# Kernel tuning notes

Measured on AMD Instinct MI355X. Metric: run time of the kernel, lower is better.

The kernel has to match this reference:

```python
import jax, jax.numpy as jnp
import numpy as np

N, E, IN_F, EDGE_F, HID, S = 200000, 600000, 28, 4, 128, 20000
NUM_LAYERS = 4
L = NUM_LAYERS - 1
BN_EPS = 1e-5


def setup_inputs() -> dict:
    key = jax.random.key(0)
    ks = jax.random.split(key, 20)
    p = lambda k, shape: (jax.random.normal(k, shape, dtype=jnp.float32) * 0.1)
    return {
        'x': jax.random.normal(ks[0], (N, IN_F), dtype=jnp.float32),
        'edge_index': jax.random.randint(ks[1], (2, E), 0, N),
        'edge_attr': jax.random.normal(ks[2], (E, EDGE_F), dtype=jnp.float32),
        'edge_weight': jax.random.uniform(ks[3], (E,), dtype=jnp.float32),
        'node_mask': (jax.random.uniform(ks[4], (N,)) > 0.5).astype(jnp.float32),
        'subgraphs2nodes': jax.random.randint(ks[5], (N,), 0, S),
        # layer-1 params (in_features -> hidden)
        'be1_W1': p(ks[6], (EDGE_F, IN_F)), 'be1_b1': jnp.zeros((IN_F,), jnp.float32),
        'be1_W2': p(ks[7], (IN_F, IN_F)), 'be1_b2': jnp.zeros((IN_F,), jnp.float32),
        'm1_W1': p(ks[8], (IN_F, HID)), 'm1_b1': jnp.zeros((HID,), jnp.float32),
        'm1_W2': p(ks[9], (HID, HID)), 'm1_b2': jnp.zeros((HID,), jnp.float32),
        'bn1_g': jnp.ones((HID,), jnp.float32), 'bn1_b': jnp.zeros((HID,), jnp.float32),
        'eps1': jnp.zeros((), jnp.float32),
        # layers 2..NUM_LAYERS, stacked (hidden -> hidden)
        'beW1': p(ks[10], (L, EDGE_F, HID)), 'beb1': jnp.zeros((L, HID), jnp.float32),
        'beW2': p(ks[11], (L, HID, HID)), 'beb2': jnp.zeros((L, HID), jnp.float32),
        'mW1': p(ks[12], (L, HID, HID)), 'mb1': jnp.zeros((L, HID), jnp.float32),
        'mW2': p(ks[13], (L, HID, HID)), 'mb2': jnp.zeros((L, HID), jnp.float32),
        'bng': jnp.ones((L, HID), jnp.float32), 'bnb': jnp.zeros((L, HID), jnp.float32),
        'eps': jnp.zeros((L,), jnp.float32),
    }


def _mlp2(h, W1, b1, W2, b2):
    # Linear -> ReLU -> Linear
    return jnp.dot(jax.nn.relu(jnp.dot(h, W1) + b1), W2) + b2


def _gine(x, src, dst, edge_attr, edge_weight, eps,
          beW1, beb1, beW2, beb2, W1, b1, W2, b2, g, beta):
    # bond encoder on edge features
    e = _mlp2(edge_attr, beW1, beb1, beW2, beb2)            # [E, d]
    # message: relu(x_j + e_ij) * w_ij, aggregated at dst via scatter-add
    m = jax.nn.relu(x[src] + e) * edge_weight[:, None]      # [E, d]
    aggr = jax.ops.segment_sum(m, dst, num_segments=N)      # [N, d]
    h = (1.0 + eps) * x + aggr
    # node MLP: Linear,ReLU,Linear,BN(train mode),ReLU
    h = _mlp2(h, W1, b1, W2, b2)
    mu = jnp.mean(h, axis=0)
    var = jnp.mean((h - mu) ** 2, axis=0)
    h = (h - mu) * jax.lax.rsqrt(var + BN_EPS) * g + beta
    return jax.nn.relu(h)


def reference(x, edge_index, edge_attr, edge_weight, node_mask, subgraphs2nodes,
              be1_W1, be1_b1, be1_W2, be1_b2, m1_W1, m1_b1, m1_W2, m1_b2,
              bn1_g, bn1_b, eps1,
              beW1, beb1, beW2, beb2, mW1, mb1, mW2, mb2, bng, bnb, eps):
    src, dst = edge_index[0], edge_index[1]
    h = _gine(x, src, dst, edge_attr, edge_weight, eps1,
              be1_W1, be1_b1, be1_W2, be1_b2,
              m1_W1, m1_b1, m1_W2, m1_b2, bn1_g, bn1_b)
    for i in range(L):
        h_new = _gine(h, src, dst, edge_attr, edge_weight, eps[i],
                      beW1[i], beb1[i], beW2[i], beb2[i],
                      mW1[i], mb1[i], mW2[i], mb2[i], bng[i], bnb[i])
        h = h + h_new  # residual
    # float node_mask branch + global_add_pool over subgraphs2nodes
    h = h * node_mask[:, None]
    return jax.ops.segment_sum(h, subgraphs2nodes, num_segments=S)  # [S, HID]
```

## Files before the change

kernel.cpp:

```cpp
#include <hip/hip_runtime.h>
#include <hip/hip_bf16.h>


#define BNEPS 1e-5f
#define LDA 136
#define SCAN_NB 240

typedef __attribute__((ext_vector_type(8))) short bf16x8;
typedef __attribute__((ext_vector_type(8))) unsigned short u16x8;
typedef __attribute__((ext_vector_type(4))) float f32x4;

__device__ inline short f2bf(float f) {
    __hip_bfloat16 h = __float2bfloat16(f);
    return *reinterpret_cast<short*>(&h);
}
__device__ inline unsigned short f2bfu(float f) {
    __hip_bfloat16 h = __float2bfloat16(f);
    return *reinterpret_cast<unsigned short*>(&h);
}
__device__ inline float bf2f(unsigned short u) {
    union { unsigned int i; float f; } v; v.i = ((unsigned int)u) << 16; return v.f;
}


__global__ __launch_bounds__(256) void k_prep(
    const float* __restrict__ m1W2, const float* __restrict__ beW2,
    const float* __restrict__ mW1, const float* __restrict__ mW2,
    short* __restrict__ out)
{
    __shared__ float tileS[64][65];
    int b = blockIdx.x, mat = b >> 2, t = b & 3;
    const float* Wsrc;
    if (mat == 0) Wsrc = m1W2;
    else {
        int l = (mat - 1) / 3, which = (mat - 1) % 3;
        Wsrc = (which == 0) ? beW2 + (size_t)l * 16384
             : (which == 1) ? mW1 + (size_t)l * 16384
             :                mW2 + (size_t)l * 16384;
    }
    short* dst = out + (size_t)mat * 16384;
    int tr = (t >> 1) * 64, tc = (t & 1) * 64;
    for (int i = threadIdx.x; i < 4096; i += 256) {
        int r = i >> 6, c = i & 63;
        tileS[r][c] = Wsrc[(size_t)(tr + r) * 128 + (tc + c)];
    }
    __syncthreads();
    for (int i = threadIdx.x; i < 4096; i += 256) {
        int kl = i & 63, nl = i >> 6;
        int n = tc + nl, k = tr + kl;
        int fo = (((n >> 4) * 4 + (k >> 5)) * 64 + (((k >> 3) & 3) * 16 + (n & 15))) * 8 + (k & 7);
        dst[fo] = f2bf(tileS[kl][nl]);
    }
}

__global__ __launch_bounds__(256) void k_prep1(
    const float* __restrict__ W1, short* __restrict__ out)
{
    for (int i = threadIdx.x; i < 4096; i += 256) {
        int j = i & 7, sub = (i >> 3) & 63, nt = i >> 9;
        int quad = sub >> 4, l15 = sub & 15;
        int n = nt * 16 + l15, k = quad * 8 + j;
        out[i] = (k < 28) ? f2bf(W1[(size_t)k * 128 + n]) : (short)0;
    }
}

__global__ __launch_bounds__(256) void k_prep28(
    const float* __restrict__ W2, short* __restrict__ out)
{
    for (int i = threadIdx.x; i < 32 * 32; i += 256) {
        int n = i >> 5, k = i & 31;
        out[i] = (n < 28 && k < 28) ? f2bf(W2[(size_t)k * 28 + n]) : (short)0;
    }
}

__global__ __launch_bounds__(256) void k_prepx(
    const float* __restrict__ x, unsigned short* __restrict__ xbf, int N)
{
    int total = N * 32;
    for (int i = blockIdx.x * 256 + threadIdx.x; i < total; i += gridDim.x * 256) {
        int n = i >> 5, c = i & 31;
        xbf[i] = (c < 28) ? f2bfu(x[(size_t)n * 28 + c]) : (unsigned short)0;
    }
}

__global__ __launch_bounds__(256) void k_count(
    const int* __restrict__ ei, int* __restrict__ counts, int E)
{
    for (int e = blockIdx.x * 256 + threadIdx.x; e < E; e += gridDim.x * 256)
        atomicAdd(&counts[ei[E + e]], 1);
}

__global__ __launch_bounds__(256) void k_count2(
    const int* __restrict__ s2n, const float* __restrict__ mask,
    int* __restrict__ counts2, int N)
{
    for (int n = blockIdx.x * 256 + threadIdx.x; n < N; n += gridDim.x * 256)
        if (mask[n] != 0.f) atomicAdd(&counts2[s2n[n]], 1);
}

__global__ __launch_bounds__(256) void k_scanA(
    const int* __restrict__ counts, int* __restrict__ bsum, int N, int seg)
{
    __shared__ int red[256];
    int b = blockIdx.x;
    int lo = b * seg, hi = min(lo + seg, N);
    int s = 0;
    for (int i = lo + threadIdx.x; i < hi; i += 256) s += counts[i];
    red[threadIdx.x] = s;
    __syncthreads();
    for (int d = 128; d > 0; d >>= 1) {
        if (threadIdx.x < d) red[threadIdx.x] += red[threadIdx.x + d];
        __syncthreads();
    }
    if (threadIdx.x == 0) bsum[b] = red[0];
}

__global__ __launch_bounds__(256) void k_scanB(
    int* __restrict__ bsum, int nb, int* __restrict__ offs, int N)
{
    __shared__ int sh[256];
    int v = (threadIdx.x < nb) ? bsum[threadIdx.x] : 0;
    sh[threadIdx.x] = v;
    __syncthreads();
    for (int d = 1; d < 256; d <<= 1) {
        int t = (threadIdx.x >= d) ? sh[threadIdx.x - d] : 0;
        __syncthreads();
        sh[threadIdx.x] += t;
        __syncthreads();
    }
    if (threadIdx.x < nb) bsum[threadIdx.x] = sh[threadIdx.x] - v;
    if (threadIdx.x == 0) offs[N] = sh[255];
}

__global__ __launch_bounds__(256) void k_scanC(
    const int* __restrict__ counts, const int* __restrict__ bsum,
    int* __restrict__ offs, int* __restrict__ cursor, int N, int seg)
{
    __shared__ int sh[256];
    int b = blockIdx.x;
    int lo = b * seg, hi = min(lo + seg, N);
    int base = bsum[b];
    for (int t0 = lo; t0 < hi; t0 += 256) {
        int i = t0 + threadIdx.x;
        int v = (i < hi) ? counts[i] : 0;
        sh[threadIdx.x] = v;
        __syncthreads();
        for (int d = 1; d < 256; d <<= 1) {
            int t = (threadIdx.x >= d) ? sh[threadIdx.x - d] : 0;
            __syncthreads();
            sh[threadIdx.x] += t;
            __syncthreads();
        }
        int excl = base + sh[threadIdx.x] - v;
        if (i < hi) { offs[i] = excl; cursor[i] = excl; }
        int tileTotal = sh[255];
        __syncthreads();
        base += tileTotal;
    }
}

__global__ __launch_bounds__(256) void k_scatter(
    const int* __restrict__ ei, const float* __restrict__ ew,
    const float4* __restrict__ ea4,
    int* __restrict__ cursor, int2* __restrict__ pmeta,
    float4* __restrict__ pea4, int E)
{
    for (int e = blockIdx.x * 256 + threadIdx.x; e < E; e += gridDim.x * 256) {
        int d = ei[E + e];
        int pos = atomicAdd(&cursor[d], 1);
        pmeta[pos] = make_int2(ei[e], __float_as_int(ew[e]));
        pea4[pos] = ea4[e];
    }
}

__global__ __launch_bounds__(256) void k_scatter2(
    const int* __restrict__ s2n, const float* __restrict__ mask,
    int* __restrict__ cursor2, int* __restrict__ perm2, int N)
{
    for (int n = blockIdx.x * 256 + threadIdx.x; n < N; n += gridDim.x * 256)
        if (mask[n] != 0.f) {
            int pos = atomicAdd(&cursor2[s2n[n]], 1);
            perm2[pos] = n;
        }
}

__global__ __launch_bounds__(256, 3) void k_emsg(
    const float4* __restrict__ pea4,
    const float* __restrict__ W1, const float* __restrict__ b1,
    const short* __restrict__ W2f, const float* __restrict__ b2,
    unsigned short* __restrict__ emsg, const int* __restrict__ offs,
    int n0, int n1)
{
    __shared__ short As[64 * LDA];
    __shared__ short Bs[16384];
    int e0 = offs[n0], e1 = offs[n1];
    int tid = threadIdx.x;
    int w = tid >> 6, lane = tid & 63;
    int l15 = lane & 15, quad = lane >> 4;
    int rb = w * 16;
    for (int i = tid; i < 2048; i += 256)
        *(bf16x8*)&Bs[i * 8] = *(const bf16x8*)&W2f[i * 8];
    int c2 = lane * 2;
    float w1a[4], w1b[4];
    #pragma unroll
    for (int a = 0; a < 4; ++a) { w1a[a] = W1[a * 128 + c2]; w1b[a] = W1[a * 128 + c2 + 1]; }
    float b1a = b1[c2], b1b = b1[c2 + 1];
    float b2r[8];
    #pragma unroll
    for (int nt = 0; nt < 8; ++nt) b2r[nt] = b2[nt * 16 + l15];
    __syncthreads();

    const float* peaf = (const float*)pea4;
    int numTiles = (e1 - e0 + 63) >> 6;
    for (int tile = blockIdx.x; tile < numTiles; tile += gridDim.x) {
        int base = e0 + tile * 64;
        int eidx = base + rb + (lane >> 2);
        float v = (eidx < e1) ? peaf[(size_t)(base + rb) * 4 + lane] : 0.f;
        #pragma unroll
        for (int e = 0; e < 16; ++e) {
            float a0v = __shfl(v, e * 4 + 0);
            float a1v = __shfl(v, e * 4 + 1);
            float a2v = __shfl(v, e * 4 + 2);
            float a3v = __shfl(v, e * 4 + 3);
            float t0 = fmaf(a0v, w1a[0], fmaf(a1v, w1a[1], fmaf(a2v, w1a[2], fmaf(a3v, w1a[3], b1a))));
            float t1 = fmaf(a0v, w1b[0], fmaf(a1v, w1b[1], fmaf(a2v, w1b[2], fmaf(a3v, w1b[3], b1b))));
            unsigned int pk = ((unsigned int)f2bfu(fmaxf(t1, 0.f)) << 16) | f2bfu(fmaxf(t0, 0.f));
        *(unsigned int*)&As[(rb + e) * LDA + c2] = pk;
        }
        f32x4 acc[8];
        #pragma unroll
        for (int nt = 0; nt < 8; ++nt) acc[nt] = (f32x4){0.f, 0.f, 0.f, 0.f};
        #pragma unroll
        for (int kt = 0; kt < 4; ++kt) {
            bf16x8 af = *(bf16x8*)&As[(rb + l15) * LDA + kt * 32 + quad * 8];
            #pragma unroll
            for (int nt = 0; nt < 8; ++nt) {
                bf16x8 bf = *(const bf16x8*)&Bs[((nt * 4 + kt) * 64 + lane) * 8];
                acc[nt] = __builtin_amdgcn_mfma_f32_16x16x32_bf16(af, bf, acc[nt], 0, 0, 0);
            }
        }
        #pragma unroll
        for (int nt = 0; nt < 8; ++nt) {
            #pragma unroll
            for (int r = 0; r < 4; ++r)
                As[(rb + quad * 4 + r) * LDA + nt * 16 + l15] = f2bf(acc[nt][r] + b2r[nt]);
        }
        #pragma unroll
        for (int it = 0; it < 4; ++it) {
            int arow = rb + it * 4 + quad;
            int gr = base + arow;
            if (gr < e1)
                *(bf16x8*)&emsg[(size_t)(gr - e0) * 128 + l15 * 8] = *(bf16x8*)&As[arow * LDA + l15 * 8];
        }
    }
}

__global__ __launch_bounds__(256) void k_emsg28_mm(
    const float4* __restrict__ pea4,
    const float* __restrict__ W1, const float* __restrict__ b1,
    const short* __restrict__ W2t28,
    const float* __restrict__ b2,
    unsigned short* __restrict__ emsg28, int E)
{
    __shared__ short Bs[32 * 40];
    __shared__ short As[64 * 40];
    __shared__ float eas[64][4];
    __shared__ float b2s[32];
    int tid = threadIdx.x;
    for (int i = tid; i < 32 * 32; i += 256) {
        int n = i >> 5, k = i & 31;
        Bs[n * 40 + k] = W2t28[i];
    }
    if (tid < 32) b2s[tid] = (tid < 28) ? b2[tid] : 0.f;
    int j = tid & 31, sub = tid >> 5;
    float w10 = 0.f, w11 = 0.f, w12 = 0.f, w13 = 0.f, b1j = 0.f;
    if (j < 28) { w10 = W1[j]; w11 = W1[28 + j]; w12 = W1[56 + j]; w13 = W1[84 + j]; b1j = b1[j]; }
    int w = tid >> 6, lane = tid & 63;
    int l15 = lane & 15, quad = lane >> 4;
    __syncthreads();

    int numTiles = (E + 63) >> 6;
    for (int tile = blockIdx.x; tile < numTiles; tile += gridDim.x) {
        int base = tile * 64;
        __syncthreads();
        if (tid < 64) {
            int k = base + tid;
            float4 a = (k < E) ? pea4[k] : make_float4(0.f, 0.f, 0.f, 0.f);
            eas[tid][0] = a.x; eas[tid][1] = a.y; eas[tid][2] = a.z; eas[tid][3] = a.w;
        }
        __syncthreads();
        #pragma unroll
        for (int q = 0; q < 8; ++q) {
            int e = q * 8 + sub;
            float t = fmaf(eas[e][0], w10, fmaf(eas[e][1], w11,
                      fmaf(eas[e][2], w12, fmaf(eas[e][3], w13, b1j))));
            As[e * 40 + j] = (j < 28) ? f2bf(fmaxf(t, 0.f)) : (short)0;
        }
        __syncthreads();
        f32x4 acc[2];
        acc[0] = (f32x4){0.f, 0.f, 0.f, 0.f};
        acc[1] = (f32x4){0.f, 0.f, 0.f, 0.f};
        bf16x8 af = *(bf16x8*)&As[(w * 16 + l15) * 40 + quad * 8];
        #pragma unroll
        for (int nt = 0; nt < 2; ++nt) {
            bf16x8 bf = *(bf16x8*)&Bs[(nt * 16 + l15) * 40 + quad * 8];
            acc[nt] = __builtin_amdgcn_mfma_f32_16x16x32_bf16(af, bf, acc[nt], 0, 0, 0);
        }
        __syncthreads();
        #pragma unroll
        for (int nt = 0; nt < 2; ++nt) {
            int col = nt * 16 + l15;
            float bb = b2s[col];
            #pragma unroll
            for (int r = 0; r < 4; ++r)
                As[(w * 16 + quad * 4 + r) * 40 + col] = f2bf(acc[nt][r] + bb);
        }
        __syncthreads();
        for (int i = tid; i < 64 * 28; i += 256) {
            int row = i / 28, col = i - row * 28;
            int gr = base + row;
            if (gr < E) emsg28[(size_t)gr * 28 + col] = As[row * 40 + col];
        }
    }
}

__global__ __launch_bounds__(256) void k_gather(
    const unsigned short* __restrict__ h, const int* __restrict__ offs,
    const int2* __restrict__ pmeta, const unsigned short* __restrict__ emsg,
    unsigned short* __restrict__ a0,
    const float* __restrict__ epsp, int epsIdx,
    int n0, int n1)
{
    int grp = threadIdx.x >> 5, lane = threadIdx.x & 31;
    int n = n0 + blockIdx.x * 8 + grp;
    if (n >= n1) return;
    int e0 = offs[n0];
    int k0 = offs[n], k1 = offs[n + 1];
    float s = 1.0f + epsp[epsIdx];
    ushort4 hv0 = *(const ushort4*)&h[(size_t)n * 128 + lane * 4];
    float m0 = s * bf2f(hv0.x), m1 = s * bf2f(hv0.y);
    float m2 = s * bf2f(hv0.z), m3 = s * bf2f(hv0.w);
    for (int k = k0; k < k1; ++k) {
        int2 mt = pmeta[k];
        float w = __int_as_float(mt.y);
        ushort4 ev = *(const ushort4*)&emsg[(size_t)(k - e0) * 128 + lane * 4];
        ushort4 hv = *(const ushort4*)&h[(size_t)mt.x * 128 + lane * 4];
        m0 += fmaxf(bf2f(hv.x) + bf2f(ev.x), 0.f) * w;
        m1 += fmaxf(bf2f(hv.y) + bf2f(ev.y), 0.f) * w;
        m2 += fmaxf(bf2f(hv.z) + bf2f(ev.z), 0.f) * w;
        m3 += fmaxf(bf2f(hv.w) + bf2f(ev.w), 0.f) * w;
    }
    ushort4 o;
    o.x = f2bfu(m0); o.y = f2bfu(m1); o.z = f2bfu(m2); o.w = f2bfu(m3);
    *(ushort4*)&a0[(size_t)n * 128 + lane * 4] = o;
}

__global__ __launch_bounds__(256) void k_gather28(
    const float* __restrict__ x, const unsigned short* __restrict__ xbf,
    const int* __restrict__ offs,
    const int2* __restrict__ pmeta, const unsigned short* __restrict__ emsg28,
    const float* __restrict__ eps1, float* __restrict__ u28, int N)
{
    int grp = threadIdx.x >> 5, lane = threadIdx.x & 31;
    int n = blockIdx.x * 8 + grp;
    if (n >= N || lane >= 28) return;
    float s = 1.0f + eps1[0];
    int k0 = offs[n], k1 = offs[n + 1];
    float m = 0.f;
    for (int k = k0; k < k1; ++k) {
        int2 mt = pmeta[k];
        float w = __int_as_float(mt.y);
        float e = bf2f(emsg28[(size_t)k * 28 + lane]);
        float xs = bf2f(xbf[(size_t)mt.x * 32 + lane]);
        m += fmaxf(xs + e, 0.f) * w;
    }
    u28[(size_t)n * 28 + lane] = fmaf(s, x[(size_t)n * 28 + lane], m);
}

__global__ __launch_bounds__(512, 2) void k_mlp(
    const unsigned short* __restrict__ src, const short* __restrict__ W1f,
    const float* __restrict__ b1, const short* __restrict__ W2f,
    const float* __restrict__ b2, unsigned short* __restrict__ dst,
    float* __restrict__ stats, int N)
{
    __shared__ short As[256 * LDA];
    __shared__ short Bs1[16384];
    __shared__ short Bs2[16384];
    __shared__ float sstat[256];
    int tid = threadIdx.x;
    for (int i = tid; i < 2048; i += 512) {
        *(bf16x8*)&Bs1[i * 8] = *(const bf16x8*)&W1f[i * 8];
        *(bf16x8*)&Bs2[i * 8] = *(const bf16x8*)&W2f[i * 8];
    }
    if (tid < 256) sstat[tid] = 0.f;
    int w = tid >> 6, lane = tid & 63;
    int l15 = lane & 15, quad = lane >> 4;
    int rb = w * 32;
    float b1r[8], b2r[8], lsum[8], lsq[8];
    #pragma unroll
    for (int nt = 0; nt < 8; ++nt) {
        b1r[nt] = b1[nt * 16 + l15]; b2r[nt] = b2[nt * 16 + l15];
        lsum[nt] = 0.f; lsq[nt] = 0.f;
    }
    int numTiles = (N + 255) >> 8;
    bf16x8 st[8];
    {
        int tile = blockIdx.x;
        if (tile < numTiles) {
            int base = tile * 256;
            #pragma unroll
            for (int kk = 0; kk < 8; ++kk) {
                int i = tid + kk * 512;
                int rr = base + (i >> 4);
                st[kk] = (rr < N) ? *(const bf16x8*)&src[(size_t)rr * 128 + (i & 15) * 8]
                                  : (bf16x8){0, 0, 0, 0, 0, 0, 0, 0};
            }
        }
    }
    __syncthreads();

    for (int tile = blockIdx.x; tile < numTiles; tile += gridDim.x) {
        int base = tile * 256;
        #pragma unroll
        for (int kk = 0; kk < 8; ++kk) {
            int i = tid + kk * 512;
            *(bf16x8*)&As[(i >> 4) * LDA + (i & 15) * 8] = st[kk];
        }
        int tnext = tile + gridDim.x;
        if (tnext < numTiles) {
            int bn = tnext * 256;
            #pragma unroll
            for (int kk = 0; kk < 8; ++kk) {
                int i = tid + kk * 512;
                int rr = bn + (i >> 4);
                st[kk] = (rr < N) ? *(const bf16x8*)&src[(size_t)rr * 128 + (i & 15) * 8]
                                  : (bf16x8){0, 0, 0, 0, 0, 0, 0, 0};
            }
        }
        __syncthreads();
        f32x4 acc[2][8];
        #pragma unroll
        for (int rg = 0; rg < 2; ++rg)
            #pragma unroll
            for (int nt = 0; nt < 8; ++nt) acc[rg][nt] = (f32x4){0.f, 0.f, 0.f, 0.f};
        #pragma unroll
        for (int kt = 0; kt < 4; ++kt) {
            bf16x8 af0 = *(bf16x8*)&As[(rb + l15) * LDA + kt * 32 + quad * 8];
            bf16x8 af1 = *(bf16x8*)&As[(rb + 16 + l15) * LDA + kt * 32 + quad * 8];
            #pragma unroll
            for (int nt = 0; nt < 8; ++nt) {
                bf16x8 bf = *(const bf16x8*)&Bs1[((nt * 4 + kt) * 64 + lane) * 8];
                acc[0][nt] = __builtin_amdgcn_mfma_f32_16x16x32_bf16(af0, bf, acc[0][nt], 0, 0, 0);
                acc[1][nt] = __builtin_amdgcn_mfma_f32_16x16x32_bf16(af1, bf, acc[1][nt], 0, 0, 0);
            }
        }
        #pragma unroll
        for (int rg = 0; rg < 2; ++rg)
            #pragma unroll
            for (int nt = 0; nt < 8; ++nt)
                #pragma unroll
                for (int r = 0; r < 4; ++r)
                    As[(rb + rg * 16 + quad * 4 + r) * LDA + nt * 16 + l15] =
                        f2bf(fmaxf(acc[rg][nt][r] + b1r[nt], 0.f));
        #pragma unroll
        for (int rg = 0; rg < 2; ++rg)
            #pragma unroll
            for (int nt = 0; nt < 8; ++nt) acc[rg][nt] = (f32x4){0.f, 0.f, 0.f, 0.f};
        #pragma unroll
        for (int kt = 0; kt < 4; ++kt) {
            bf16x8 af0 = *(bf16x8*)&As[(rb + l15) * LDA + kt * 32 + quad * 8];
            bf16x8 af1 = *(bf16x8*)&As[(rb + 16 + l15) * LDA + kt * 32 + quad * 8];
            #pragma unroll
            for (int nt = 0; nt < 8; ++nt) {
                bf16x8 bf = *(const bf16x8*)&Bs2[((nt * 4 + kt) * 64 + lane) * 8];
                acc[0][nt] = __builtin_amdgcn_mfma_f32_16x16x32_bf16(af0, bf, acc[0][nt], 0, 0, 0);
                acc[1][nt] = __builtin_amdgcn_mfma_f32_16x16x32_bf16(af1, bf, acc[1][nt], 0, 0, 0);
            }
        }
        #pragma unroll
        for (int rg = 0; rg < 2; ++rg)
            #pragma unroll
            for (int nt = 0; nt < 8; ++nt) {
                int row0 = base + rb + rg * 16 + quad * 4;
                #pragma unroll
                for (int r = 0; r < 4; ++r) {
                    float z = acc[rg][nt][r] + b2r[nt];
                    if (row0 + r < N) { lsum[nt] += z; lsq[nt] = fmaf(z, z, lsq[nt]); }
                    As[(rb + rg * 16 + quad * 4 + r) * LDA + nt * 16 + l15] = f2bf(z);
                }
            }
        #pragma unroll
        for (int it = 0; it < 8; ++it) {
            int arow = rb + it * 4 + quad;
            int rr = base + arow;
            if (rr < N)
                *(bf16x8*)&dst[(size_t)rr * 128 + l15 * 8] = *(bf16x8*)&As[arow * LDA + l15 * 8];
        }
        __syncthreads();
    }
    #pragma unroll
    for (int nt = 0; nt < 8; ++nt) {
        atomicAdd(&sstat[nt * 16 + l15], lsum[nt]);
        atomicAdd(&sstat[128 + nt * 16 + l15], lsq[nt]);
    }
    __syncthreads();
    if (tid < 256) atomicAdd(&stats[tid], sstat[tid]);
}

__global__ __launch_bounds__(512, 2) void k_mlp1(
    const float* __restrict__ u28, const short* __restrict__ W1f,
    const float* __restrict__ b1, const short* __restrict__ W2f,
    const float* __restrict__ b2, unsigned short* __restrict__ dst,
    float* __restrict__ stats, int N)
{
    __shared__ short A28[256 * 40];
    __shared__ short As[256 * LDA];
    __shared__ short Bs1[4096];
    __shared__ short Bs2[16384];
    __shared__ float sstat[256];
    int tid = threadIdx.x;
    if (tid < 512) {
        int i = tid;
        *(bf16x8*)&Bs1[i * 8] = *(const bf16x8*)&W1f[i * 8];
    }
    for (int i = tid; i < 2048; i += 512)
        *(bf16x8*)&Bs2[i * 8] = *(const bf16x8*)&W2f[i * 8];
    for (int i = tid; i < 1024; i += 512) {
        int row = i >> 2, c = 28 + (i & 3);
        A28[row * 40 + c] = 0;
    }
    if (tid < 256) sstat[tid] = 0.f;
    int w = tid >> 6, lane = tid & 63;
    int l15 = lane & 15, quad = lane >> 4;
    int rb = w * 32;
    float b1r[8], b2r[8], lsum[8], lsq[8];
    #pragma unroll
    for (int nt = 0; nt < 8; ++nt) {
        b1r[nt] = b1[nt * 16 + l15]; b2r[nt] = b2[nt * 16 + l15];
        lsum[nt] = 0.f; lsq[nt] = 0.f;
    }
    int numTiles = (N + 255) >> 8;
    float stf[14];
    {
        int tile = blockIdx.x;
        if (tile < numTiles) {
            int base = tile * 256;
            #pragma unroll
            for (int kk = 0; kk < 14; ++kk) {
                int idx = tid + kk * 512;
                int row = idx / 28, col = idx - row * 28;
                int rr = base + row;
                stf[kk] = (rr < N) ? u28[(size_t)rr * 28 + col] : 0.f;
            }
        }
    }
    __syncthreads();

    for (int tile = blockIdx.x; tile < numTiles; tile += gridDim.x) {
        int base = tile * 256;
        #pragma unroll
        for (int kk = 0; kk < 14; ++kk) {
            int idx = tid + kk * 512;
            int row = idx / 28, col = idx - row * 28;
            A28[row * 40 + col] = f2bf(stf[kk]);
        }
        int tnext = tile + gridDim.x;
        if (tnext < numTiles) {
            int bn = tnext * 256;
            #pragma unroll
            for (int kk = 0; kk < 14; ++kk) {
                int idx = tid + kk * 512;
                int row = idx / 28, col = idx - row * 28;
                int rr = bn + row;
                stf[kk] = (rr < N) ? u28[(size_t)rr * 28 + col] : 0.f;
            }
        }
        __syncthreads();
        f32x4 acc[2][8];
        #pragma unroll
        for (int rg = 0; rg < 2; ++rg)
            #pragma unroll
            for (int nt = 0; nt < 8; ++nt) acc[rg][nt] = (f32x4){0.f, 0.f, 0.f, 0.f};
        {
            bf16x8 af0 = *(bf16x8*)&A28[(rb + l15) * 40 + quad * 8];
            bf16x8 af1 = *(bf16x8*)&A28[(rb + 16 + l15) * 40 + quad * 8];
            #pragma unroll
            for (int nt = 0; nt < 8; ++nt) {
                bf16x8 bf = *(const bf16x8*)&Bs1[(nt * 64 + lane) * 8];
                acc[0][nt] = __builtin_amdgcn_mfma_f32_16x16x32_bf16(af0, bf, acc[0][nt], 0, 0, 0);
                acc[1][nt] = __builtin_amdgcn_mfma_f32_16x16x32_bf16(af1, bf, acc[1][nt], 0, 0, 0);
            }
        }
        #pragma unroll
        for (int rg = 0; rg < 2; ++rg)
            #pragma unroll
            for (int nt = 0; nt < 8; ++nt)
                #pragma unroll
                for (int r = 0; r < 4; ++r)
                    As[(rb + rg * 16 + quad * 4 + r) * LDA + nt * 16 + l15] =
                        f2bf(fmaxf(acc[rg][nt][r] + b1r[nt], 0.f));
        #pragma unroll
        for (int rg = 0; rg < 2; ++rg)
            #pragma unroll
            for (int nt = 0; nt < 8; ++nt) acc[rg][nt] = (f32x4){0.f, 0.f, 0.f, 0.f};
        #pragma unroll
        for (int kt = 0; kt < 4; ++kt) {
            bf16x8 af0 = *(bf16x8*)&As[(rb + l15) * LDA + kt * 32 + quad * 8];
            bf16x8 af1 = *(bf16x8*)&As[(rb + 16 + l15) * LDA + kt * 32 + quad * 8];
            #pragma unroll
            for (int nt = 0; nt < 8; ++nt) {
                bf16x8 bf = *(const bf16x8*)&Bs2[((nt * 4 + kt) * 64 + lane) * 8];
                acc[0][nt] = __builtin_amdgcn_mfma_f32_16x16x32_bf16(af0, bf, acc[0][nt], 0, 0, 0);
                acc[1][nt] = __builtin_amdgcn_mfma_f32_16x16x32_bf16(af1, bf, acc[1][nt], 0, 0, 0);
            }
        }
        #pragma unroll
        for (int rg = 0; rg < 2; ++rg)
            #pragma unroll
            for (int nt = 0; nt < 8; ++nt) {
                int row0 = base + rb + rg * 16 + quad * 4;
                #pragma unroll
                for (int r = 0; r < 4; ++r) {
                    float z = acc[rg][nt][r] + b2r[nt];
                    if (row0 + r < N) { lsum[nt] += z; lsq[nt] = fmaf(z, z, lsq[nt]); }
                    As[(rb + rg * 16 + quad * 4 + r) * LDA + nt * 16 + l15] = f2bf(z);
                }
            }
        #pragma unroll
        for (int it = 0; it < 8; ++it) {
            int arow = rb + it * 4 + quad;
            int rr = base + arow;
            if (rr < N)
                *(bf16x8*)&dst[(size_t)rr * 128 + l15 * 8] = *(bf16x8*)&As[arow * LDA + l15 * 8];
        }
        __syncthreads();
    }
    #pragma unroll
    for (int nt = 0; nt < 8; ++nt) {
        atomicAdd(&sstat[nt * 16 + l15], lsum[nt]);
        atomicAdd(&sstat[128 + nt * 16 + l15], lsq[nt]);
    }
    __syncthreads();
    if (tid < 256) atomicAdd(&stats[tid], sstat[tid]);
}

__global__ __launch_bounds__(128) void k_stats(
    const float* __restrict__ stats, const float* __restrict__ g,
    const float* __restrict__ b, float* __restrict__ ss, float invN)
{
    int j = threadIdx.x;
    float mu  = stats[j] * invN;
    float var = fmaf(stats[128 + j], invN, -mu * mu);
    float sc  = rsqrtf(fmaxf(var, 0.f) + BNEPS) * g[j];
    ss[j] = sc;
    ss[128 + j] = fmaf(-mu, sc, b[j]);
}

__global__ __launch_bounds__(256) void k_bn(
    const unsigned short* __restrict__ z, const float* __restrict__ ss,
    unsigned short* __restrict__ h, int residual, int N)
{
    int idx8 = blockIdx.x * 256 + threadIdx.x;
    int stride = gridDim.x * 256;
    int c0 = (idx8 & 15) * 8;
    float scl[8], sht[8];
    #pragma unroll
    for (int r = 0; r < 8; ++r) { scl[r] = ss[c0 + r]; sht[r] = ss[128 + c0 + r]; }
    int total8 = N * 16;
    for (; idx8 < total8; idx8 += stride) {
        int n = idx8 >> 4;
        u16x8 z8 = *(const u16x8*)&z[(size_t)n * 128 + c0];
        float hn[8];
        #pragma unroll
        for (int r = 0; r < 8; ++r)
            hn[r] = fmaxf(fmaf(bf2f(z8[r]), scl[r], sht[r]), 0.f);
        if (residual) {
            u16x8 h8 = *(const u16x8*)&h[(size_t)n * 128 + c0];
            #pragma unroll
            for (int r = 0; r < 8; ++r) hn[r] += bf2f(h8[r]);
        }
        u16x8 o;
        #pragma unroll
        for (int r = 0; r < 8; ++r) o[r] = f2bfu(hn[r]);
        *(u16x8*)&h[(size_t)n * 128 + c0] = o;
    }
}

__global__ __launch_bounds__(256) void k_poolbn(
    const unsigned short* __restrict__ z, const unsigned short* __restrict__ hprev,
    const float* __restrict__ ss, const int* __restrict__ offs2,
    const int* __restrict__ perm2, float* __restrict__ out, int S)
{
    int w = threadIdx.x >> 6, lane = threadIdx.x & 63;
    int s = blockIdx.x * 4 + w;
    if (s >= S) return;
    int c0 = lane * 2;
    float scl0 = ss[c0], scl1 = ss[c0 + 1];
    float sht0 = ss[128 + c0], sht1 = ss[128 + c0 + 1];
    int k0 = offs2[s], k1 = offs2[s + 1];
    float a0 = 0.f, a1 = 0.f;
    for (int k = k0; k < k1; ++k) {
        int n = perm2[k];
        ushort2 zv = *(const ushort2*)&z[(size_t)n * 128 + c0];
        ushort2 hv = *(const ushort2*)&hprev[(size_t)n * 128 + c0];
        a0 += fmaxf(fmaf(bf2f(zv.x), scl0, sht0), 0.f) + bf2f(hv.x);
        a1 += fmaxf(fmaf(bf2f(zv.y), scl1, sht1), 0.f) + bf2f(hv.y);
    }
    *(float2*)&out[(size_t)s * 128 + c0] = make_float2(a0, a1);
}

extern "C" void kernel_launch(void* const* d_in, const int* in_sizes, int n_in,
                              void* d_out, int out_size, void* d_ws, size_t ws_size,
                              hipStream_t stream) {
    const float* x    = (const float*)d_in[0];
    const int*   ei   = (const int*)d_in[1];
    const float* ea   = (const float*)d_in[2];
    const float* ew   = (const float*)d_in[3];
    const float* mask = (const float*)d_in[4];
    const int*   s2n  = (const int*)d_in[5];
    const float* be1W1 = (const float*)d_in[6];
    const float* be1b1 = (const float*)d_in[7];
    const float* be1W2 = (const float*)d_in[8];
    const float* be1b2 = (const float*)d_in[9];
    const float* m1W1  = (const float*)d_in[10];
    const float* m1b1  = (const float*)d_in[11];
    const float* m1W2  = (const float*)d_in[12];
    const float* m1b2  = (const float*)d_in[13];
    const float* bn1g  = (const float*)d_in[14];
    const float* bn1b  = (const float*)d_in[15];
    const float* eps1  = (const float*)d_in[16];
    const float* beW1  = (const float*)d_in[17];
    const float* beb1  = (const float*)d_in[18];
    const float* beW2  = (const float*)d_in[19];
    const float* beb2  = (const float*)d_in[20];
    const float* mW1   = (const float*)d_in[21];
    const float* mb1   = (const float*)d_in[22];
    const float* mW2   = (const float*)d_in[23];
    const float* mb2   = (const float*)d_in[24];
    const float* bng   = (const float*)d_in[25];
    const float* bnb   = (const float*)d_in[26];
    const float* epsL  = (const float*)d_in[27];

    const int N = in_sizes[0] / 28;
    const int E = in_sizes[1] / 2;
    const int S = out_size / 128;
    const float invN = 1.0f / (float)N;
    const int NS = N / 2;
    const int EMC = E / 2 + 8192;

    auto al16 = [](size_t v) { return (v + 15) & ~(size_t)15; };
    char* ws = (char*)d_ws;
    size_t offH      = 0;
    size_t offA0     = al16(offH + (size_t)N * 256);
    size_t offEm     = al16(offA0 + (size_t)N * 256);
    size_t emBytes   = (size_t)EMC * 256;
    if ((size_t)E * 56 > emBytes) emBytes = (size_t)E * 56;
    size_t offStats  = al16(offEm + emBytes);
    size_t offSS     = al16(offStats + 4096);
    size_t offWts    = al16(offSS + 1024);
    size_t offCounts = al16(offWts + 10 * 16384 * 2 + 4096 * 2 + 1024 * 2);
    size_t offOffs   = al16(offCounts + (size_t)N * 4);
    size_t offCursor = al16(offOffs + (size_t)(N + 1) * 4);
    size_t offPmeta  = al16(offCursor + (size_t)N * 4);
    size_t offPea    = al16(offPmeta + (size_t)E * 8);
    size_t offBsum   = al16(offPea + (size_t)E * 16);
    size_t offCnt2   = al16(offBsum + SCAN_NB * 4);
    size_t offOffs2  = al16(offCnt2 + (size_t)S * 4);
    size_t offCur2   = al16(offOffs2 + (size_t)(S + 1) * 4);
    size_t offPerm2  = al16(offCur2 + (size_t)S * 4);
    size_t need      = offPerm2 + (size_t)N * 4;
    if (ws_size < need) return;

    unsigned short* h    = (unsigned short*)(ws + offH);
    unsigned short* a0   = (unsigned short*)(ws + offA0);
    unsigned short* emsg = (unsigned short*)(ws + offEm);
    float* u28    = (float*)(ws + offA0);
    unsigned short* xbf = (unsigned short*)(ws + offA0 + 26214400);
    float* stats  = (float*)(ws + offStats);
    float* ssbuf  = (float*)(ws + offSS);
    short* wts    = (short*)(ws + offWts);
    short* w1p    = wts + 10 * 16384;
    short* w2p28  = w1p + 4096;
    int*   counts = (int*)(ws + offCounts);
    int*   offs   = (int*)(ws + offOffs);
    int*   cursor = (int*)(ws + offCursor);
    int2*  pmeta  = (int2*)(ws + offPmeta);
    float4* pea4  = (float4*)(ws + offPea);
    int*   bsum   = (int*)(ws + offBsum);
    int*   cnt2   = (int*)(ws + offCnt2);
    int*   offs2  = (int*)(ws + offOffs2);
    int*   cur2   = (int*)(ws + offCur2);
    int*   perm2  = (int*)(ws + offPerm2);
    const float4* ea4 = (const float4*)ea;

    hipMemsetAsync(stats, 0, 4 * 256 * sizeof(float), stream);
    hipMemsetAsync(counts, 0, (size_t)N * sizeof(int), stream);
    hipMemsetAsync(cnt2, 0, (size_t)S * sizeof(int), stream);

    k_prep<<<40, 256, 0, stream>>>(m1W2, beW2, mW1, mW2, wts);
    k_prep1<<<1, 256, 0, stream>>>(m1W1, w1p);
    k_prep28<<<1, 256, 0, stream>>>(be1W2, w2p28);
    k_prepx<<<512, 256, 0, stream>>>(x, xbf, N);

    const int seg = (N + SCAN_NB - 1) / SCAN_NB;
    k_count<<<1024, 256, 0, stream>>>(ei, counts, E);
    k_scanA<<<SCAN_NB, 256, 0, stream>>>(counts, bsum, N, seg);
    k_scanB<<<1, 256, 0, stream>>>(bsum, SCAN_NB, offs, N);
    k_scanC<<<SCAN_NB, 256, 0, stream>>>(counts, bsum, offs, cursor, N, seg);
    k_scatter<<<1024, 256, 0, stream>>>(ei, ew, ea4, cursor, pmeta, pea4, E);

    const int seg2 = (S + SCAN_NB - 1) / SCAN_NB;
    k_count2<<<512, 256, 0, stream>>>(s2n, mask, cnt2, N);
    k_scanA<<<SCAN_NB, 256, 0, stream>>>(cnt2, bsum, S, seg2);
    k_scanB<<<1, 256, 0, stream>>>(bsum, SCAN_NB, offs2, S);
    k_scanC<<<SCAN_NB, 256, 0, stream>>>(cnt2, bsum, offs2, cur2, S, seg2);
    k_scatter2<<<512, 256, 0, stream>>>(s2n, mask, cur2, perm2, N);

    auto wt_be = [&](int l) { return wts + (size_t)(1 + 3 * l + 0) * 16384; };
    auto wt_m1 = [&](int l) { return wts + (size_t)(1 + 3 * l + 1) * 16384; };
    auto wt_m2 = [&](int l) { return wts + (size_t)(1 + 3 * l + 2) * 16384; };

    k_emsg28_mm<<<2048, 256, 0, stream>>>(pea4, be1W1, be1b1, w2p28, be1b2, emsg, E);
    k_gather28<<<(N + 7) / 8, 256, 0, stream>>>(x, xbf, offs, pmeta, emsg, eps1, u28, N);
    k_mlp1<<<256, 512, 0, stream>>>(u28, w1p, m1b1, wts , m1b2, h, stats, N);
    k_stats<<<1, 128, 0, stream>>>(stats, bn1g, bn1b, ssbuf, invN);
    k_bn<<<2048, 256, 0, stream>>>(h, ssbuf, h, 0, N);

    for (int l = 0; l < 3; ++l) {
        for (int c = 0; c < 2; ++c) {
            int n0 = (c == 0) ? 0 : NS;
            int n1 = (c == 0) ? NS : N;
            k_emsg<<<2048, 256, 0, stream>>>(pea4,
                beW1 + (size_t)l * 512, beb1 + (size_t)l * 128,
                wt_be(l), beb2 + (size_t)l * 128, emsg, offs, n0, n1);
            k_gather<<<(n1 - n0 + 7) / 8, 256, 0, stream>>>(h, offs, pmeta, emsg, a0,
                epsL, l, n0, n1);
        }
        k_mlp<<<256, 512, 0, stream>>>(a0, wt_m1(l), mb1 + (size_t)l * 128,
                                       wt_m2(l), mb2 + (size_t)l * 128, a0,
                                       stats + 256 * (l + 1), N);
        k_stats<<<1, 128, 0, stream>>>(stats + 256 * (l + 1),
            bng + (size_t)l * 128, bnb + (size_t)l * 128, ssbuf, invN);
        if (l < 2) {
            k_bn<<<2048, 256, 0, stream>>>(a0, ssbuf, h, 1, N);
        }
    }

    k_poolbn<<<(S + 3) / 4, 256, 0, stream>>>(a0, h, ssbuf, offs2, perm2,
                                              (float*)d_out, S);
}
```

Measured before the change: 1.030 ms.

## Merge weight-prep kernels, rewrite 28-wide edge MLP barrier-free, prefetch gather loads

Folds the two small weight-prep kernels into the main prep kernel as extra blocks, saving two launches. Rewrites the 28-wide edge-encoder kernel so each wave holds its B fragments in registers, computes the first layer with shuffles, and writes vectorized output without block-wide barriers. Adds two-deep software prefetching of the edge metadata, edge message and source-node rows in both gather kernels, to hide dependent global-load latency. The prefetch costs extra registers, and the new fragment layout for the 28x28 weight has to match the MFMA operand order.

Result: no change. 1.035 ms (+0.5%).

```diff
diff --git a/kernel.cpp b/kernel.cpp
--- a/kernel.cpp
+++ b/kernel.cpp
@@ -26,10 +26,30 @@
 __global__ __launch_bounds__(256) void k_prep(
     const float* __restrict__ m1W2, const float* __restrict__ beW2,
     const float* __restrict__ mW1, const float* __restrict__ mW2,
-    short* __restrict__ out)
+    const float* __restrict__ m1W1, const float* __restrict__ be1W2,
+    short* __restrict__ out, short* __restrict__ out1, short* __restrict__ out28)
 {
     __shared__ float tileS[64][65];
-    int b = blockIdx.x, mat = b >> 2, t = b & 3;
+    int b = blockIdx.x;
+    if (b == 40) {
+        for (int i = threadIdx.x; i < 4096; i += 256) {
+            int j = i & 7, sub = (i >> 3) & 63, nt = i >> 9;
+            int quad = sub >> 4, l15 = sub & 15;
+            int n = nt * 16 + l15, k = quad * 8 + j;
+            out1[i] = (k < 28) ? f2bf(m1W1[(size_t)k * 128 + n]) : (short)0;
+        }
+        return;
+    }
+    if (b == 41) {
+        for (int i = threadIdx.x; i < 1024; i += 256) {
+            int j = i & 7, lane = (i >> 3) & 63, nt = i >> 9;
+            int quad = lane >> 4, l15 = lane & 15;
+            int n = nt * 16 + l15, k = quad * 8 + j;
+            out28[i] = (n < 28 && k < 28) ? f2bf(be1W2[(size_t)k * 28 + n]) : (short)0;
+        }
+        return;
+    }
+    int mat = b >> 2, t = b & 3;
     const float* Wsrc;
     if (mat == 0) Wsrc = m1W2;
     else {
@@ -50,26 +70,6 @@
         int n = tc + nl, k = tr + kl;
         int fo = (((n >> 4) * 4 + (k >> 5)) * 64 + (((k >> 3) & 3) * 16 + (n & 15))) * 8 + (k & 7);
         dst[fo] = f2bf(tileS[kl][nl]);
-    }
-}
-
-__global__ __launch_bounds__(256) void k_prep1(
-    const float* __restrict__ W1, short* __restrict__ out)
-{
-    for (int i = threadIdx.x; i < 4096; i += 256) {
-        int j = i & 7, sub = (i >> 3) & 63, nt = i >> 9;
-        int quad = sub >> 4, l15 = sub & 15;
-        int n = nt * 16 + l15, k = quad * 8 + j;
-        out[i] = (k < 28) ? f2bf(W1[(size_t)k * 128 + n]) : (short)0;
-    }
-}
-
-__global__ __launch_bounds__(256) void k_prep28(
-    const float* __restrict__ W2, short* __restrict__ out)
-{
-    for (int i = threadIdx.x; i < 32 * 32; i += 256) {
-        int n = i >> 5, k = i & 31;
-        out[i] = (n < 28 && k < 28) ? f2bf(W2[(size_t)k * 28 + n]) : (short)0;
     }
 }
 
@@ -225,7 +225,7 @@
             float t0 = fmaf(a0v, w1a[0], fmaf(a1v, w1a[1], fmaf(a2v, w1a[2], fmaf(a3v, w1a[3], b1a))));
             float t1 = fmaf(a0v, w1b[0], fmaf(a1v, w1b[1], fmaf(a2v, w1b[2], fmaf(a3v, w1b[3], b1b))));
             unsigned int pk = ((unsigned int)f2bfu(fmaxf(t1, 0.f)) << 16) | f2bfu(fmaxf(t0, 0.f));
-        *(unsigned int*)&As[(rb + e) * LDA + c2] = pk;
+            *(unsigned int*)&As[(rb + e) * LDA + c2] = pk;
         }
         f32x4 acc[8];
         #pragma unroll
@@ -255,71 +255,67 @@
     }
 }
 
-__global__ __launch_bounds__(256) void k_emsg28_mm(
+__global__ __launch_bounds__(256, 4) void k_emsg28_mm(
     const float4* __restrict__ pea4,
     const float* __restrict__ W1, const float* __restrict__ b1,
-    const short* __restrict__ W2t28,
+    const short* __restrict__ W2f28,
     const float* __restrict__ b2,
     unsigned short* __restrict__ emsg28, int E)
 {
-    __shared__ short Bs[32 * 40];
     __shared__ short As[64 * 40];
-    __shared__ float eas[64][4];
-    __shared__ float b2s[32];
     int tid = threadIdx.x;
-    for (int i = tid; i < 32 * 32; i += 256) {
-        int n = i >> 5, k = i & 31;
-        Bs[n * 40 + k] = W2t28[i];
-    }
-    if (tid < 32) b2s[tid] = (tid < 28) ? b2[tid] : 0.f;
-    int j = tid & 31, sub = tid >> 5;
-    float w10 = 0.f, w11 = 0.f, w12 = 0.f, w13 = 0.f, b1j = 0.f;
-    if (j < 28) { w10 = W1[j]; w11 = W1[28 + j]; w12 = W1[56 + j]; w13 = W1[84 + j]; b1j = b1[j]; }
     int w = tid >> 6, lane = tid & 63;
     int l15 = lane & 15, quad = lane >> 4;
-    __syncthreads();
-
+    int rb = w * 16;
+    bf16x8 B0 = *(const bf16x8*)&W2f28[(size_t)lane * 8];
+    bf16x8 B1 = *(const bf16x8*)&W2f28[(size_t)(64 + lane) * 8];
+    int c2 = l15 * 2;
+    bool act = (c2 < 28);
+    float w1a[4], w1b[4], b1a, b1b;
+    #pragma unroll
+    for (int a = 0; a < 4; ++a) {
+        w1a[a] = act ? W1[a * 28 + c2] : 0.f;
+        w1b[a] = act ? W1[a * 28 + c2 + 1] : 0.f;
+    }
+    b1a = act ? b1[c2] : 0.f;
+    b1b = act ? b1[c2 + 1] : 0.f;
+    float b2r0 = b2[l15];
+    float b2r1 = (l15 < 12) ? b2[16 + l15] : 0.f;
+
+    const float* peaf = (const float*)pea4;
     int numTiles = (E + 63) >> 6;
     for (int tile = blockIdx.x; tile < numTiles; tile += gridDim.x) {
         int base = tile * 64;
-        __syncthreads();
-        if (tid < 64) {
-            int k = base + tid;
-            float4 a = (k < E) ? pea4[k] : make_float4(0.f, 0.f, 0.f, 0.f);
-            eas[tid][0] = a.x; eas[tid][1] = a.y; eas[tid][2] = a.z; eas[tid][3] = a.w;
-        }
-        __syncthreads();
-        #pragma unroll
-        for (int q = 0; q < 8; ++q) {
-            int e = q * 8 + sub;
-            float t = fmaf(eas[e][0], w10, fmaf(eas[e][1], w11,
-                      fmaf(eas[e][2], w12, fmaf(eas[e][3], w13, b1j))));
-            As[e * 40 + j] = (j < 28) ? f2bf(fmaxf(t, 0.f)) : (short)0;
-        }
-        __syncthreads();
-        f32x4 acc[2];
-        acc[0] = (f32x4){0.f, 0.f, 0.f, 0.f};
-        acc[1] = (f32x4){0.f, 0.f, 0.f, 0.f};
-        bf16x8 af = *(bf16x8*)&As[(w * 16 + l15) * 40 + quad * 8];
-        #pragma unroll
-        for (int nt = 0; nt < 2; ++nt) {
-            bf16x8 bf = *(bf16x8*)&Bs[(nt * 16 + l15) * 40 + quad * 8];
-            acc[nt] = __builtin_amdgcn_mfma_f32_16x16x32_bf16(af, bf, acc[nt], 0, 0, 0);
-        }
-        __syncthreads();
-        #pragma unroll
-        for (int nt = 0; nt < 2; ++nt) {
-            int col = nt * 16 + l15;
-            float bb = b2s[col];
-            #pragma unroll
-            for (int r = 0; r < 4; ++r)
-                As[(w * 16 + quad * 4 + r) * 40 + col] = f2bf(acc[nt][r] + bb);
-        }
-        __syncthreads();
-        for (int i = tid; i < 64 * 28; i += 256) {
-            int row = i / 28, col = i - row * 28;
-            int gr = base + row;
-            if (gr < E) emsg28[(size_t)gr * 28 + col] = As[row * 40 + col];
+        int eidx = base + rb + (lane >> 2);
+        float v = (eidx < E) ? peaf[(size_t)(base + rb) * 4 + lane] : 0.f;
+        #pragma unroll
+        for (int e = 0; e < 16; ++e) {
+            float a0v = __shfl(v, e * 4 + 0);
+            float a1v = __shfl(v, e * 4 + 1);
+            float a2v = __shfl(v, e * 4 + 2);
+            float a3v = __shfl(v, e * 4 + 3);
+            float t0 = fmaf(a0v, w1a[0], fmaf(a1v, w1a[1], fmaf(a2v, w1a[2], fmaf(a3v, w1a[3], b1a))));
+            float t1 = fmaf(a0v, w1b[0], fmaf(a1v, w1b[1], fmaf(a2v, w1b[2], fmaf(a3v, w1b[3], b1b))));
+            unsigned int pk = ((unsigned int)f2bfu(fmaxf(t1, 0.f)) << 16) | f2bfu(fmaxf(t0, 0.f));
+            if (quad == (e & 3))
+                *(unsigned int*)&As[(rb + e) * 40 + c2] = pk;
+        }
+        f32x4 acc0 = (f32x4){0.f, 0.f, 0.f, 0.f};
+        f32x4 acc1 = (f32x4){0.f, 0.f, 0.f, 0.f};
+        bf16x8 af = *(bf16x8*)&As[(rb + l15) * 40 + quad * 8];
+        acc0 = __builtin_amdgcn_mfma_f32_16x16x32_bf16(af, B0, acc0, 0, 0, 0);
+        acc1 = __builtin_amdgcn_mfma_f32_16x16x32_bf16(af, B1, acc1, 0, 0, 0);
+        #pragma unroll
+        for (int r = 0; r < 4; ++r) {
+            As[(rb + quad * 4 + r) * 40 + l15] = f2bf(acc0[r] + b2r0);
+            As[(rb + quad * 4 + r) * 40 + 16 + l15] = f2bf(acc1[r] + b2r1);
+        }
+        #pragma unroll
+        for (int it = 0; it < 4; ++it) {
+            int arow = rb + it * 4 + quad;
+            int gr = base + arow;
+            if (gr < E && l15 < 14)
+                *(ushort2*)&emsg28[(size_t)gr * 28 + c2] = *(ushort2*)&As[arow * 40 + c2];
         }
     }
 }
@@ -340,15 +336,30 @@
     ushort4 hv0 = *(const ushort4*)&h[(size_t)n * 128 + lane * 4];
     float m0 = s * bf2f(hv0.x), m1 = s * bf2f(hv0.y);
     float m2 = s * bf2f(hv0.z), m3 = s * bf2f(hv0.w);
+    int2 mtA, mtB;
+    ushort4 evA, hvA, evB, hvB;
+    if (k0 < k1) {
+        mtA = pmeta[k0];
+        evA = *(const ushort4*)&emsg[(size_t)(k0 - e0) * 128 + lane * 4];
+        hvA = *(const ushort4*)&h[(size_t)mtA.x * 128 + lane * 4];
+    }
+    if (k0 + 1 < k1) {
+        mtB = pmeta[k0 + 1];
+        evB = *(const ushort4*)&emsg[(size_t)(k0 + 1 - e0) * 128 + lane * 4];
+        hvB = *(const ushort4*)&h[(size_t)mtB.x * 128 + lane * 4];
+    }
     for (int k = k0; k < k1; ++k) {
-        int2 mt = pmeta[k];
-        float w = __int_as_float(mt.y);
-        ushort4 ev = *(const ushort4*)&emsg[(size_t)(k - e0) * 128 + lane * 4];
-        ushort4 hv = *(const ushort4*)&h[(size_t)mt.x * 128 + lane * 4];
-        m0 += fmaxf(bf2f(hv.x) + bf2f(ev.x), 0.f) * w;
-        m1 += fmaxf(bf2f(hv.y) + bf2f(ev.y), 0.f) * w;
-        m2 += fmaxf(bf2f(hv.z) + bf2f(ev.z), 0.f) * w;
-        m3 += fmaxf(bf2f(hv.w) + bf2f(ev.w), 0.f) * w;
+        float w = __int_as_float(mtA.y);
+        m0 += fmaxf(bf2f(hvA.x) + bf2f(evA.x), 0.f) * w;
+        m1 += fmaxf(bf2f(hvA.y) + bf2f(evA.y), 0.f) * w;
+        m2 += fmaxf(bf2f(hvA.z) + bf2f(evA.z), 0.f) * w;
+        m3 += fmaxf(bf2f(hvA.w) + bf2f(evA.w), 0.f) * w;
+        mtA = mtB; evA = evB; hvA = hvB;
+        if (k + 2 < k1) {
+            mtB = pmeta[k + 2];
+            evB = *(const ushort4*)&emsg[(size_t)(k + 2 - e0) * 128 + lane * 4];
+            hvB = *(const ushort4*)&h[(size_t)mtB.x * 128 + lane * 4];
+        }
     }
     ushort4 o;
     o.x = f2bfu(m0); o.y = f2bfu(m1); o.z = f2bfu(m2); o.w = f2bfu(m3);
@@ -367,12 +378,27 @@
     float s = 1.0f + eps1[0];
     int k0 = offs[n], k1 = offs[n + 1];
     float m = 0.f;
+    int2 mtA, mtB;
+    unsigned short eA = 0, xA = 0, eB = 0, xB = 0;
+    if (k0 < k1) {
+        mtA = pmeta[k0];
+        eA = emsg28[(size_t)k0 * 28 + lane];
+        xA = xbf[(size_t)mtA.x * 32 + lane];
+    }
+    if (k0 + 1 < k1) {
+        mtB = pmeta[k0 + 1];
+        eB = emsg28[(size_t)(k0 + 1) * 28 + lane];
+        xB = xbf[(size_t)mtB.x * 32 + lane];
+    }
     for (int k = k0; k < k1; ++k) {
-        int2 mt = pmeta[k];
-        float w = __int_as_float(mt.y);
-        float e = bf2f(emsg28[(size_t)k * 28 + lane]);
-        float xs = bf2f(xbf[(size_t)mt.x * 32 + lane]);
-        m += fmaxf(xs + e, 0.f) * w;
+        float w = __int_as_float(mtA.y);
+        m += fmaxf(bf2f(xA) + bf2f(eA), 0.f) * w;
+        mtA = mtB; eA = eB; xA = xB;
+        if (k + 2 < k1) {
+            mtB = pmeta[k + 2];
+            eB = emsg28[(size_t)(k + 2) * 28 + lane];
+            xB = xbf[(size_t)mtB.x * 32 + lane];
+        }
     }
     u28[(size_t)n * 28 + lane] = fmaf(s, x[(size_t)n * 28 + lane], m);
 }
@@ -797,9 +823,7 @@
     hipMemsetAsync(counts, 0, (size_t)N * sizeof(int), stream);
     hipMemsetAsync(cnt2, 0, (size_t)S * sizeof(int), stream);
 
-    k_prep<<<40, 256, 0, stream>>>(m1W2, beW2, mW1, mW2, wts);
-    k_prep1<<<1, 256, 0, stream>>>(m1W1, w1p);
-    k_prep28<<<1, 256, 0, stream>>>(be1W2, w2p28);
+    k_prep<<<42, 256, 0, stream>>>(m1W2, beW2, mW1, mW2, m1W1, be1W2, wts, w1p, w2p28);
     k_prepx<<<512, 256, 0, stream>>>(x, xbf, N);
 
     const int seg = (N + SCAN_NB - 1) / SCAN_NB;
```
